# Kernel optimization log

Measured on AMD Instinct MI355X. Metric: run time of the kernel, lower is better.

The kernel has to match this reference:

```python
import jax, jax.numpy as jnp
import numpy as np

B, L, D, H = 4, 2048, 1024, 16
DH = D // H
EPS = 1e-6

def layer_norm(x, g, b):
    mu = jnp.mean(x, axis=-1, keepdims=True)
    var = jnp.mean(jnp.square(x - mu), axis=-1, keepdims=True)
    return (x - mu) * jax.lax.rsqrt(var + EPS) * g + b

def setup_inputs() -> dict:
    key = jax.random.key(0)
    ks = jax.random.split(key, 8)
    s = 0.02
    return {
        "x": jax.random.normal(ks[0], (B, L, D), jnp.float32),
        "mask": jnp.ones((B, L), jnp.int32),
        "Wq": jax.random.normal(ks[1], (D, D), jnp.float32) * s,
        "bq": jnp.zeros((D,), jnp.float32),
        "Wk": jax.random.normal(ks[2], (D, D), jnp.float32) * s,
        "bk": jnp.zeros((D,), jnp.float32),
        "Wv": jax.random.normal(ks[3], (D, D), jnp.float32) * s,
        "bv": jnp.zeros((D,), jnp.float32),
        "g1": jnp.ones((D,), jnp.float32),
        "b1": jnp.zeros((D,), jnp.float32),
        "g2": jnp.ones((D,), jnp.float32),
        "b2": jnp.zeros((D,), jnp.float32),
        "Wo1": jax.random.normal(ks[4], (D, D), jnp.float32) * s,
        "bo1": jnp.zeros((D,), jnp.float32),
        "Wo2": jax.random.normal(ks[5], (D, D), jnp.float32) * s,
        "bo2": jnp.zeros((D,), jnp.float32),
    }

def reference(x, mask, Wq, bq, Wk, bk, Wv, bv, g1, b1, g2, b2, Wo1, bo1, Wo2, bo2):
    h = layer_norm(x, g1, b1)                                  # [B,L,D]
    q = (h @ Wq + bq).reshape(B, L, H, DH)
    k = (h @ Wk + bk).reshape(B, L, H, DH)
    v = (h @ Wv + bv).reshape(B, L, H, DH)
    scores = jnp.einsum('bqhd,bkhd->bhqk', q, k) / jnp.sqrt(jnp.float32(DH))
    m = mask.astype(scores.dtype)[:, None, None, :]            # [B,1,1,L]
    scores = scores + (1.0 - m) * (-1e30)                      # mask_logits
    probs = jax.nn.softmax(scores, axis=-1)
    attn = jnp.einsum('bhqk,bkhd->bqhd', probs, v).reshape(B, L, D)
    residual = x + attn
    out = layer_norm(residual, g2, b2)
    out = jax.nn.gelu(out @ Wo1 + bo1, approximate=False)      # exact GELU (nn.GELU)
    out = out @ Wo2 + bo2 + residual
    return out
```

## Files before the change

kernel.cpp:

```cpp
#include <hip/hip_runtime.h>
#include <stdint.h>
#include <math.h>

typedef __bf16 bf16_t;
typedef __bf16 bf16x8 __attribute__((ext_vector_type(8)));
typedef __bf16 bf16x4 __attribute__((ext_vector_type(4)));
typedef float f32x4 __attribute__((ext_vector_type(4)));

#define B_ 4
#define L_ 2048
#define D_ 1024
#define H_ 16
#define DH_ 64
#define M_ (B_ * L_)
#define QSCALE 0.18033688011112042f

__device__ __forceinline__ void gload16(const bf16_t* gsrc, bf16_t* ldst) {
    __builtin_amdgcn_global_load_lds(
        (__attribute__((address_space(1))) void*)(void*)(gsrc),
        (__attribute__((address_space(3))) void*)(ldst), 16, 0, 0);
}

__device__ __forceinline__ float gelu_exact(float v) {
    return 0.5f * v * (1.0f + erff(v * 0.70710678118654752f));
}

__device__ __forceinline__ float fast_exp2(float x) {
#if __has_builtin(__builtin_amdgcn_exp2f)
    return __builtin_amdgcn_exp2f(x);
#else
    return exp2f(x);
#endif
}

__global__ __launch_bounds__(256) void transpose5(const float* __restrict__ W0, const float* __restrict__ W1,
                                                  const float* __restrict__ W2, const float* __restrict__ W3,
                                                  const float* __restrict__ W4,
                                                  bf16_t* __restrict__ T0, bf16_t* __restrict__ T1,
                                                  bf16_t* __restrict__ T2, bf16_t* __restrict__ T3,
                                                  bf16_t* __restrict__ T4) {
    const float* W; bf16_t* T;
    switch (blockIdx.z) {
        case 0: W = W0; T = T0; break;
        case 1: W = W1; T = T1; break;
        case 2: W = W2; T = T2; break;
        case 3: W = W3; T = T3; break;
        default: W = W4; T = T4; break;
    }
    __shared__ float tile[32][33];
    const int x = threadIdx.x, y0 = threadIdx.y;
    const int bx = blockIdx.x * 32, by = blockIdx.y * 32;
    for (int kk = 0; kk < 4; ++kk)
        tile[y0 + kk * 8][x] = W[(size_t)(by + y0 + kk * 8) * D_ + bx + x];
    __syncthreads();
    for (int kk = 0; kk < 4; ++kk)
        T[(size_t)(bx + y0 + kk * 8) * D_ + by + x] = (bf16_t)tile[x][y0 + kk * 8];
}

__global__ __launch_bounds__(256) void maskbias_kernel(const int* __restrict__ mask,
                                                       float* __restrict__ mb,
                                                       unsigned char* __restrict__ flags) {
    const int i = blockIdx.x * 256 + threadIdx.x;
    const int m = mask[i];
    mb[i] = m ? 0.f : -1.0e30f;
    const unsigned long long bal = __ballot(m != 0);
    __shared__ unsigned char ok[4];
    if ((threadIdx.x & 63) == 0) ok[threadIdx.x >> 6] = (bal == ~0ull) ? 1 : 0;
    __syncthreads();
    if (threadIdx.x < 2)
        flags[blockIdx.x * 2 + threadIdx.x] =
            (unsigned char)(ok[threadIdx.x * 2] & ok[threadIdx.x * 2 + 1]);
}

#define VTR_STRIDE 76
__global__ __launch_bounds__(256) void vtrans_kernel(const bf16_t* __restrict__ vb,
                                                     bf16_t* __restrict__ vt) {
    __shared__ bf16_t tile[128 * VTR_STRIDE];
    const int t = threadIdx.x;
    const int bh = blockIdx.y, b = bh >> 4, h = bh & 15;
    const int k0 = blockIdx.x * 128;
    #pragma unroll
    for (int it = 0; it < 4; ++it) {
        const int row = it * 32 + (t >> 3), c8 = (t & 7) * 8;
        *(uint4*)&tile[row * VTR_STRIDE + c8] =
            *(const uint4*)(vb + (size_t)(b * L_ + k0 + row) * D_ + h * DH_ + c8);
    }
    __syncthreads();
    #pragma unroll
    for (int it = 0; it < 4; ++it) {
        const int d = it * 16 + (t >> 4), pos0 = (t & 15) * 8;
        const int base32 = pos0 & ~31, g = (pos0 >> 3) & 3;
        union { uint4 u; bf16_t e[8]; } tv;
        #pragma unroll
        for (int j = 0; j < 8; ++j) {
            const int kk = base32 + ((j >> 2) << 4) + (g << 2) + (j & 3);
            tv.e[j] = tile[kk * VTR_STRIDE + d];
        }
        *(uint4*)&vt[((size_t)bh * DH_ + d) * L_ + k0 + pos0] = tv.u;
    }
}

__global__ __launch_bounds__(256) void ln1_kernel(const float* __restrict__ x,
                                                  const float* __restrict__ g,
                                                  const float* __restrict__ b,
                                                  bf16_t* __restrict__ h) {
    const int row = blockIdx.x, t = threadIdx.x;
    const float4 v = *(const float4*)(x + (size_t)row * D_ + t * 4);
    float s = v.x + v.y + v.z + v.w;
    float s2 = v.x * v.x + v.y * v.y + v.z * v.z + v.w * v.w;
    for (int m = 1; m < 64; m <<= 1) { s += __shfl_xor(s, m, 64); s2 += __shfl_xor(s2, m, 64); }
    __shared__ float red[2][4];
    if ((t & 63) == 0) { red[0][t >> 6] = s; red[1][t >> 6] = s2; }
    __syncthreads();
    s = red[0][0] + red[0][1] + red[0][2] + red[0][3];
    s2 = red[1][0] + red[1][1] + red[1][2] + red[1][3];
    const float mean = s * (1.f / 1024.f);
    const float var = s2 * (1.f / 1024.f) - mean * mean;
    const float rstd = rsqrtf(var + 1e-6f);
    const float4 gv = *(const float4*)(g + t * 4);
    const float4 bv = *(const float4*)(b + t * 4);
    union { bf16_t h4[4]; uint2 u; } o;
    o.h4[0] = (bf16_t)((v.x - mean) * rstd * gv.x + bv.x);
    o.h4[1] = (bf16_t)((v.y - mean) * rstd * gv.y + bv.y);
    o.h4[2] = (bf16_t)((v.z - mean) * rstd * gv.z + bv.z);
    o.h4[3] = (bf16_t)((v.w - mean) * rstd * gv.w + bv.w);
    *(uint2*)(h + (size_t)row * D_ + t * 4) = o.u;
}

__global__ __launch_bounds__(256) void add_ln2_kernel(const float* __restrict__ x,
                                                      const bf16_t* __restrict__ attnb,
                                                      const float* __restrict__ g,
                                                      const float* __restrict__ b,
                                                      bf16_t* __restrict__ residb,
                                                      bf16_t* __restrict__ h) {
    const int row = blockIdx.x, t = threadIdx.x;
    const float4 xv = *(const float4*)(x + (size_t)row * D_ + t * 4);
    union { uint2 u; bf16_t h4[4]; } ai;
    ai.u = *(const uint2*)(attnb + (size_t)row * D_ + t * 4);
    float4 v;
    v.x = xv.x + (float)ai.h4[0]; v.y = xv.y + (float)ai.h4[1];
    v.z = xv.z + (float)ai.h4[2]; v.w = xv.w + (float)ai.h4[3];
    union { bf16_t h4[4]; uint2 u; } rs;
    rs.h4[0] = (bf16_t)v.x; rs.h4[1] = (bf16_t)v.y; rs.h4[2] = (bf16_t)v.z; rs.h4[3] = (bf16_t)v.w;
    *(uint2*)(residb + (size_t)row * D_ + t * 4) = rs.u;
    float s = v.x + v.y + v.z + v.w;
    float s2 = v.x * v.x + v.y * v.y + v.z * v.z + v.w * v.w;
    for (int m = 1; m < 64; m <<= 1) { s += __shfl_xor(s, m, 64); s2 += __shfl_xor(s2, m, 64); }
    __shared__ float red[2][4];
    if ((t & 63) == 0) { red[0][t >> 6] = s; red[1][t >> 6] = s2; }
    __syncthreads();
    s = red[0][0] + red[0][1] + red[0][2] + red[0][3];
    s2 = red[1][0] + red[1][1] + red[1][2] + red[1][3];
    const float mean = s * (1.f / 1024.f);
    const float var = s2 * (1.f / 1024.f) - mean * mean;
    const float rstd = rsqrtf(var + 1e-6f);
    const float4 gv = *(const float4*)(g + t * 4);
    const float4 bv = *(const float4*)(b + t * 4);
    union { bf16_t h4[4]; uint2 u; } o;
    o.h4[0] = (bf16_t)((v.x - mean) * rstd * gv.x + bv.x);
    o.h4[1] = (bf16_t)((v.y - mean) * rstd * gv.y + bv.y);
    o.h4[2] = (bf16_t)((v.z - mean) * rstd * gv.z + bv.z);
    o.h4[3] = (bf16_t)((v.w - mean) * rstd * gv.w + bv.w);
    *(uint2*)(h + (size_t)row * D_ + t * 4) = o.u;
}

__global__ __launch_bounds__(256) void gemm_qkv(const bf16_t* __restrict__ A,
                                                const bf16_t* __restrict__ BT,
                                                const float* __restrict__ bq,
                                                const float* __restrict__ bk,
                                                const float* __restrict__ bv,
                                                bf16_t* __restrict__ qb,
                                                bf16_t* __restrict__ kb,
                                                bf16_t* __restrict__ vb) {
    constexpr int K = 1024;
    __shared__ bf16_t As[128 * 32];
    __shared__ bf16_t Bs[128 * 32];
    const int t = threadIdx.x;
    const int wave = t >> 6, lane = t & 63;
    const int l16 = lane & 15, g4 = lane >> 4;
    const int bm = blockIdx.x * 128, bn = blockIdx.y * 128;
    const int wm = (wave >> 1) * 64, wn = (wave & 1) * 64;

    f32x4 acc[4][4];
    for (int i = 0; i < 4; ++i)
        for (int j = 0; j < 4; ++j) acc[i][j] = (f32x4){0.f, 0.f, 0.f, 0.f};

    const int ar = t >> 2, ak = (t & 3) * 8;
    const bf16_t* Ag = A + (size_t)(bm + ar) * K + ak;
    const bf16_t* Bg = BT + (size_t)(bn + ar) * K + ak;
    bf16_t* Al = As + t * 8;
    bf16_t* Bl = Bs + t * 8;

    for (int kk = 0; kk < K; kk += 32) {
        __syncthreads();
        gload16(Ag + kk, Al);
        gload16(Ag + (size_t)64 * K + kk, Al + 2048);
        gload16(Bg + kk, Bl);
        gload16(Bg + (size_t)64 * K + kk, Bl + 2048);
        __syncthreads();
        bf16x8 af[4], bfr[4];
        for (int i = 0; i < 4; ++i)
            af[i] = *(const bf16x8*)&As[(wm + i * 16 + l16) * 32 + g4 * 8];
        for (int j = 0; j < 4; ++j)
            bfr[j] = *(const bf16x8*)&Bs[(wn + j * 16 + l16) * 32 + g4 * 8];
        for (int i = 0; i < 4; ++i)
            for (int j = 0; j < 4; ++j)
                acc[i][j] = __builtin_amdgcn_mfma_f32_16x16x32_bf16(af[i], bfr[j], acc[i][j], 0, 0, 0);
    }

    const int which = bn >> 10;
    const int c0 = bn & 1023;
    const float* bias = (which == 0) ? bq : (which == 1) ? bk : bv;
    bf16_t* ob = (which == 0) ? qb : (which == 1) ? kb : vb;
    const float scale = (which == 0) ? QSCALE : 1.0f;

    for (int i = 0; i < 4; ++i)
        for (int j = 0; j < 4; ++j) {
            const int col = c0 + wn + j * 16 + l16;
            const float bvv = bias[col];
            const int row0 = bm + wm + i * 16 + g4 * 4;
            for (int r = 0; r < 4; ++r) {
                const float vv = (acc[i][j][r] + bvv) * scale;
                ob[(size_t)(row0 + r) * D_ + col] = (bf16_t)vv;
            }
        }
}

template <int MODE>
__global__ __launch_bounds__(256) void gemm_bt(const bf16_t* __restrict__ A,
                                               const bf16_t* __restrict__ BT,
                                               const float* __restrict__ bias,
                                               const bf16_t* __restrict__ residb,
                                               bf16_t* __restrict__ outb,
                                               float* __restrict__ outf) {
    constexpr int K = 1024, N = 1024;
    __shared__ bf16_t As[128 * 32];
    __shared__ bf16_t Bs[128 * 32];
    const int t = threadIdx.x;
    const int wave = t >> 6, lane = t & 63;
    const int l16 = lane & 15, g4 = lane >> 4;
    const int bm = blockIdx.x * 128, bn = blockIdx.y * 128;
    const int wm = (wave >> 1) * 64, wn = (wave & 1) * 64;

    f32x4 acc[4][4];
    for (int i = 0; i < 4; ++i)
        for (int j = 0; j < 4; ++j) acc[i][j] = (f32x4){0.f, 0.f, 0.f, 0.f};

    const int ar = t >> 2, ak = (t & 3) * 8;
    const bf16_t* Ag = A + (size_t)(bm + ar) * K + ak;
    const bf16_t* Bg = BT + (size_t)(bn + ar) * K + ak;
    bf16_t* Al = As + t * 8;
    bf16_t* Bl = Bs + t * 8;

    for (int kk = 0; kk < K; kk += 32) {
        __syncthreads();
        gload16(Ag + kk, Al);
        gload16(Ag + (size_t)64 * K + kk, Al + 2048);
        gload16(Bg + kk, Bl);
        gload16(Bg + (size_t)64 * K + kk, Bl + 2048);
        __syncthreads();
        bf16x8 af[4], bfr[4];
        for (int i = 0; i < 4; ++i)
            af[i] = *(const bf16x8*)&As[(wm + i * 16 + l16) * 32 + g4 * 8];
        for (int j = 0; j < 4; ++j)
            bfr[j] = *(const bf16x8*)&Bs[(wn + j * 16 + l16) * 32 + g4 * 8];
        for (int i = 0; i < 4; ++i)
            for (int j = 0; j < 4; ++j)
                acc[i][j] = __builtin_amdgcn_mfma_f32_16x16x32_bf16(af[i], bfr[j], acc[i][j], 0, 0, 0);
    }

    for (int i = 0; i < 4; ++i)
        for (int j = 0; j < 4; ++j) {
            const int col = bn + wn + j * 16 + l16;
            const float bv = bias[col];
            const int row0 = bm + wm + i * 16 + g4 * 4;
            for (int r = 0; r < 4; ++r) {
                float vv = acc[i][j][r] + bv;
                const size_t idx = (size_t)(row0 + r) * N + col;
                if (MODE == 1) {
                    outb[idx] = (bf16_t)gelu_exact(vv);
                } else {
                    outf[idx] = vv + (float)residb[idx];
                }
            }
        }
}

#define VT_STRIDE 152
#define OS_STRIDE 72
__global__ __launch_bounds__(256, 3) void attn_kernel(const bf16_t* __restrict__ q,
                                                      const bf16_t* __restrict__ k,
                                                      const bf16_t* __restrict__ vt,
                                                      const float* __restrict__ maskbias,
                                                      const unsigned char* __restrict__ mflags,
                                                      bf16_t* __restrict__ attnb) {
    __shared__ bf16_t Ks[128 * 64];
    __shared__ bf16_t VT[64 * VT_STRIDE];
    bf16_t* Os = VT;

    const int t = threadIdx.x;
    const int wave = t >> 6, lane = t & 63;
    const int l16 = lane & 15, g4 = lane >> 4;
    const int id = blockIdx.x;
    const int xcd = id & 7, seq = id >> 3;
    const int bh = xcd * 8 + (seq >> 4);
    const int b = bh >> 4, h = bh & 15;
    const int q0 = (seq & 15) * 128;

    bf16x8 qf[2][2];
    for (int ti = 0; ti < 2; ++ti)
        for (int c = 0; c < 2; ++c)
            qf[ti][c] = *(const bf16x8*)(q + (size_t)(b * L_ + q0 + wave * 32 + ti * 16 + l16) * D_ +
                                         h * DH_ + c * 32 + g4 * 8);

    f32x4 accO[2][5];
    for (int ti = 0; ti < 2; ++ti)
        for (int dt = 0; dt < 5; ++dt) accO[ti][dt] = (f32x4){0.f, 0.f, 0.f, 0.f};

    const bf16_t ozv = (l16 == 0) ? (bf16_t)1.0f : (bf16_t)0.0f;
    const bf16x8 ones8 = (bf16x8){ozv, ozv, ozv, ozv, ozv, ozv, ozv, ozv};

    const int krow0 = t >> 3, kcg = t & 7;
    const int klcg = kcg ^ (krow0 & 7);
    const bf16_t* kbase = k + (size_t)(b * L_ + krow0) * D_ + h * DH_ + klcg * 8;
    bf16_t* kdst = Ks + t * 8;
    const int vrow0 = t >> 4, vkg = t & 15;
    const bf16_t* vbase = vt + ((size_t)bh * DH_ + vrow0) * L_ + vkg * 8;
    bf16_t* vdst = &VT[vrow0 * VT_STRIDE + vkg * 8];

    const int kb0 = l16 * 64 + ((g4 ^ (l16 & 7)) * 8);
    const int kb1 = l16 * 64 + (((g4 + 4) ^ (l16 & 7)) * 8);
    const int vrb = l16 * VT_STRIDE + g4 * 8;
    const unsigned char* flg = mflags + b * 16;

    for (int k0 = 0; k0 < L_; k0 += 128) {
        __syncthreads();
        #pragma unroll
        for (int it = 0; it < 4; ++it)
            gload16(kbase + (size_t)(k0 + it * 32) * D_, kdst + it * 2048);
        #pragma unroll
        for (int it = 0; it < 4; ++it) {
            const uint4 vv = *(const uint4*)(vbase + (size_t)(it * 16) * L_ + k0);
            *(uint4*)(vdst + it * 16 * VT_STRIDE) = vv;
        }
        __syncthreads();

        f32x4 s0[8], s1[8];
        #pragma unroll
        for (int tj = 0; tj < 8; ++tj) {
            const bf16x8 kf0 = *(const bf16x8*)&Ks[tj * 1024 + kb0];
            const bf16x8 kf1 = *(const bf16x8*)&Ks[tj * 1024 + kb1];
            f32x4 a = (f32x4){0.f, 0.f, 0.f, 0.f};
            a = __builtin_amdgcn_mfma_f32_16x16x32_bf16(kf0, qf[0][0], a, 0, 0, 0);
            a = __builtin_amdgcn_mfma_f32_16x16x32_bf16(kf1, qf[0][1], a, 0, 0, 0);
            s0[tj] = a;
            f32x4 a2 = (f32x4){0.f, 0.f, 0.f, 0.f};
            a2 = __builtin_amdgcn_mfma_f32_16x16x32_bf16(kf0, qf[1][0], a2, 0, 0, 0);
            a2 = __builtin_amdgcn_mfma_f32_16x16x32_bf16(kf1, qf[1][1], a2, 0, 0, 0);
            s1[tj] = a2;
        }

        if (!flg[k0 >> 7]) {
            #pragma unroll
            for (int tj = 0; tj < 8; ++tj) {
                const float4 mb = *(const float4*)&maskbias[b * L_ + k0 + tj * 16 + g4 * 4];
                s0[tj][0] += mb.x; s0[tj][1] += mb.y; s0[tj][2] += mb.z; s0[tj][3] += mb.w;
                s1[tj][0] += mb.x; s1[tj][1] += mb.y; s1[tj][2] += mb.z; s1[tj][3] += mb.w;
            }
        }

        bf16x8 pb0[4], pb1[4];
        #pragma unroll
        for (int c = 0; c < 4; ++c) {
            pb0[c] = (bf16x8){(bf16_t)fast_exp2(s0[2 * c][0]), (bf16_t)fast_exp2(s0[2 * c][1]),
                              (bf16_t)fast_exp2(s0[2 * c][2]), (bf16_t)fast_exp2(s0[2 * c][3]),
                              (bf16_t)fast_exp2(s0[2 * c + 1][0]), (bf16_t)fast_exp2(s0[2 * c + 1][1]),
                              (bf16_t)fast_exp2(s0[2 * c + 1][2]), (bf16_t)fast_exp2(s0[2 * c + 1][3])};
            pb1[c] = (bf16x8){(bf16_t)fast_exp2(s1[2 * c][0]), (bf16_t)fast_exp2(s1[2 * c][1]),
                              (bf16_t)fast_exp2(s1[2 * c][2]), (bf16_t)fast_exp2(s1[2 * c][3]),
                              (bf16_t)fast_exp2(s1[2 * c + 1][0]), (bf16_t)fast_exp2(s1[2 * c + 1][1]),
                              (bf16_t)fast_exp2(s1[2 * c + 1][2]), (bf16_t)fast_exp2(s1[2 * c + 1][3])};
        }

        #pragma unroll
        for (int c = 0; c < 4; ++c) {
            #pragma unroll
            for (int dt = 0; dt < 4; ++dt) {
                const bf16x8 va = *(const bf16x8*)&VT[vrb + dt * 16 * VT_STRIDE + c * 32];
                accO[0][dt] = __builtin_amdgcn_mfma_f32_16x16x32_bf16(va, pb0[c], accO[0][dt], 0, 0, 0);
                accO[1][dt] = __builtin_amdgcn_mfma_f32_16x16x32_bf16(va, pb1[c], accO[1][dt], 0, 0, 0);
            }
            accO[0][4] = __builtin_amdgcn_mfma_f32_16x16x32_bf16(ones8, pb0[c], accO[0][4], 0, 0, 0);
            accO[1][4] = __builtin_amdgcn_mfma_f32_16x16x32_bf16(ones8, pb1[c], accO[1][4], 0, 0, 0);
        }
    }

    __syncthreads();
    for (int ti = 0; ti < 2; ++ti) {
        const float lv = __shfl(accO[ti][4][0], l16, 64);
        const float rl = 1.0f / lv;
        #pragma unroll
        for (int dt = 0; dt < 4; ++dt) {
            bf16x4 o4 = (bf16x4){(bf16_t)(accO[ti][dt][0] * rl), (bf16_t)(accO[ti][dt][1] * rl),
                                 (bf16_t)(accO[ti][dt][2] * rl), (bf16_t)(accO[ti][dt][3] * rl)};
            *(bf16x4*)&Os[(wave * 32 + ti * 16 + l16) * OS_STRIDE + dt * 16 + g4 * 4] = o4;
        }
    }
    __syncthreads();
    for (int cc = 0; cc < 4; ++cc) {
        const int c2 = t + cc * 256;
        const int row = c2 >> 3, k8 = c2 & 7;
        const uint4 vv = *(const uint4*)&Os[row * OS_STRIDE + k8 * 8];
        *(uint4*)&attnb[(size_t)(b * L_ + q0 + row) * D_ + h * DH_ + k8 * 8] = vv;
    }
}

extern "C" void kernel_launch(void* const* d_in, const int* in_sizes, int n_in,
                              void* d_out, int out_size, void* d_ws, size_t ws_size,
                              hipStream_t stream) {
    const float* x    = (const float*)d_in[0];
    const int*   mask = (const int*)d_in[1];
    const float* Wq   = (const float*)d_in[2];
    const float* bq   = (const float*)d_in[3];
    const float* Wk   = (const float*)d_in[4];
    const float* bk   = (const float*)d_in[5];
    const float* Wv   = (const float*)d_in[6];
    const float* bv   = (const float*)d_in[7];
    const float* g1   = (const float*)d_in[8];
    const float* b1   = (const float*)d_in[9];
    const float* g2   = (const float*)d_in[10];
    const float* b2   = (const float*)d_in[11];
    const float* Wo1  = (const float*)d_in[12];
    const float* bo1  = (const float*)d_in[13];
    const float* Wo2  = (const float*)d_in[14];
    const float* bo2  = (const float*)d_in[15];

    char* ws = (char*)d_ws;
    const size_t MBs = 1ull << 20;
    bf16_t* WqkvT = (bf16_t*)(ws + 0 * MBs);
    bf16_t* Wo1T  = (bf16_t*)(ws + 6 * MBs);
    bf16_t* Wo2T  = (bf16_t*)(ws + 8 * MBs);
    bf16_t* h1    = (bf16_t*)(ws + 10 * MBs);
    bf16_t* vtb   = h1;
    bf16_t* qb    = (bf16_t*)(ws + 26 * MBs);
    bf16_t* kb    = (bf16_t*)(ws + 42 * MBs);
    bf16_t* vb    = (bf16_t*)(ws + 58 * MBs);
    bf16_t* attnb = (bf16_t*)(ws + 74 * MBs);
    bf16_t* residb= (bf16_t*)(ws + 90 * MBs);
    float*  mbias = (float*)(ws + 106 * MBs);
    unsigned char* mflags = (unsigned char*)(ws + 107 * MBs);
    bf16_t* h2    = qb;
    bf16_t* gact  = kb;

    transpose5<<<dim3(32, 32, 5), dim3(32, 8), 0, stream>>>(
        Wq, Wk, Wv, Wo1, Wo2,
        WqkvT, WqkvT + (size_t)D_ * D_, WqkvT + (size_t)2 * D_ * D_, Wo1T, Wo2T);

    maskbias_kernel<<<M_ / 256, 256, 0, stream>>>(mask, mbias, mflags);

    ln1_kernel<<<M_, 256, 0, stream>>>(x, g1, b1, h1);

    gemm_qkv<<<dim3(M_ / 128, 3 * D_ / 128), 256, 0, stream>>>(h1, WqkvT, bq, bk, bv, qb, kb, vb);

    vtrans_kernel<<<dim3(L_ / 128, B_ * H_), 256, 0, stream>>>(vb, vtb);

    attn_kernel<<<dim3(1024), 256, 0, stream>>>(qb, kb, vtb, mbias, mflags, attnb);

    add_ln2_kernel<<<M_, 256, 0, stream>>>(x, attnb, g2, b2, residb, h2);

    const dim3 gg(M_ / 128, D_ / 128);
    gemm_bt<1><<<gg, 256, 0, stream>>>(h2, Wo1T, bo1, nullptr, gact, nullptr);
    gemm_bt<2><<<gg, 256, 0, stream>>>(gact, Wo2T, bo2, residb, nullptr, (float*)d_out);
}
```

Before: 341.1 us.

## Merge prep kernels into one launch and swizzle attention V tile for occupancy

Folds the weight transpose, mask-bias and LN1 kernels into a single launch whose block index selects the task, removing two kernel launches and their serialization gaps. In the attention kernel, the padded V-transpose shared tile is replaced by an unpadded XOR-swizzled 128-wide layout, cutting shared memory to 32 KB. Launch bounds are raised from 3 to 4 blocks per CU to increase occupancy. The tighter register budget may cause spills, and the swizzle must keep bank conflicts low.

```diff
diff --git a/kernel.cpp b/kernel.cpp
--- a/kernel.cpp
+++ b/kernel.cpp
@@ -33,43 +33,73 @@
 #endif
 }
 
-__global__ __launch_bounds__(256) void transpose5(const float* __restrict__ W0, const float* __restrict__ W1,
-                                                  const float* __restrict__ W2, const float* __restrict__ W3,
-                                                  const float* __restrict__ W4,
-                                                  bf16_t* __restrict__ T0, bf16_t* __restrict__ T1,
-                                                  bf16_t* __restrict__ T2, bf16_t* __restrict__ T3,
-                                                  bf16_t* __restrict__ T4) {
-    const float* W; bf16_t* T;
-    switch (blockIdx.z) {
-        case 0: W = W0; T = T0; break;
-        case 1: W = W1; T = T1; break;
-        case 2: W = W2; T = T2; break;
-        case 3: W = W3; T = T3; break;
-        default: W = W4; T = T4; break;
-    }
-    __shared__ float tile[32][33];
-    const int x = threadIdx.x, y0 = threadIdx.y;
-    const int bx = blockIdx.x * 32, by = blockIdx.y * 32;
-    for (int kk = 0; kk < 4; ++kk)
-        tile[y0 + kk * 8][x] = W[(size_t)(by + y0 + kk * 8) * D_ + bx + x];
-    __syncthreads();
-    for (int kk = 0; kk < 4; ++kk)
-        T[(size_t)(bx + y0 + kk * 8) * D_ + by + x] = (bf16_t)tile[x][y0 + kk * 8];
-}
-
-__global__ __launch_bounds__(256) void maskbias_kernel(const int* __restrict__ mask,
-                                                       float* __restrict__ mb,
-                                                       unsigned char* __restrict__ flags) {
-    const int i = blockIdx.x * 256 + threadIdx.x;
-    const int m = mask[i];
-    mb[i] = m ? 0.f : -1.0e30f;
-    const unsigned long long bal = __ballot(m != 0);
-    __shared__ unsigned char ok[4];
-    if ((threadIdx.x & 63) == 0) ok[threadIdx.x >> 6] = (bal == ~0ull) ? 1 : 0;
-    __syncthreads();
-    if (threadIdx.x < 2)
-        flags[blockIdx.x * 2 + threadIdx.x] =
-            (unsigned char)(ok[threadIdx.x * 2] & ok[threadIdx.x * 2 + 1]);
+__global__ __launch_bounds__(256) void prep_kernel(const float* __restrict__ W0, const float* __restrict__ W1,
+                                                   const float* __restrict__ W2, const float* __restrict__ W3,
+                                                   const float* __restrict__ W4,
+                                                   bf16_t* __restrict__ T0, bf16_t* __restrict__ T1,
+                                                   bf16_t* __restrict__ T2, bf16_t* __restrict__ T3,
+                                                   bf16_t* __restrict__ T4,
+                                                   const int* __restrict__ mask,
+                                                   float* __restrict__ mb,
+                                                   unsigned char* __restrict__ flags,
+                                                   const float* __restrict__ x,
+                                                   const float* __restrict__ g1,
+                                                   const float* __restrict__ b1,
+                                                   bf16_t* __restrict__ h) {
+    const int z = blockIdx.x;
+    const int t = threadIdx.x;
+    if (z < 5120) {
+        const int wsel = z >> 10, tile = z & 1023;
+        const float* W; bf16_t* T;
+        switch (wsel) {
+            case 0: W = W0; T = T0; break;
+            case 1: W = W1; T = T1; break;
+            case 2: W = W2; T = T2; break;
+            case 3: W = W3; T = T3; break;
+            default: W = W4; T = T4; break;
+        }
+        __shared__ float tl[32][33];
+        const int xx = t & 31, y0 = t >> 5;
+        const int bx = (tile & 31) * 32, by = (tile >> 5) * 32;
+        for (int kk = 0; kk < 4; ++kk)
+            tl[y0 + kk * 8][xx] = W[(size_t)(by + y0 + kk * 8) * D_ + bx + xx];
+        __syncthreads();
+        for (int kk = 0; kk < 4; ++kk)
+            T[(size_t)(bx + y0 + kk * 8) * D_ + by + xx] = (bf16_t)tl[xx][y0 + kk * 8];
+    } else if (z < 5152) {
+        const int blk = z - 5120;
+        const int i = blk * 256 + t;
+        const int m = mask[i];
+        mb[i] = m ? 0.f : -1.0e30f;
+        const unsigned long long bal = __ballot(m != 0);
+        __shared__ unsigned char ok[4];
+        if ((t & 63) == 0) ok[t >> 6] = (bal == ~0ull) ? 1 : 0;
+        __syncthreads();
+        if (t < 2)
+            flags[blk * 2 + t] = (unsigned char)(ok[t * 2] & ok[t * 2 + 1]);
+    } else {
+        const int row = z - 5152;
+        const float4 v = *(const float4*)(x + (size_t)row * D_ + t * 4);
+        float s = v.x + v.y + v.z + v.w;
+        float s2 = v.x * v.x + v.y * v.y + v.z * v.z + v.w * v.w;
+        for (int m = 1; m < 64; m <<= 1) { s += __shfl_xor(s, m, 64); s2 += __shfl_xor(s2, m, 64); }
+        __shared__ float red[2][4];
+        if ((t & 63) == 0) { red[0][t >> 6] = s; red[1][t >> 6] = s2; }
+        __syncthreads();
+        s = red[0][0] + red[0][1] + red[0][2] + red[0][3];
+        s2 = red[1][0] + red[1][1] + red[1][2] + red[1][3];
+        const float mean = s * (1.f / 1024.f);
+        const float var = s2 * (1.f / 1024.f) - mean * mean;
+        const float rstd = rsqrtf(var + 1e-6f);
+        const float4 gv = *(const float4*)(g1 + t * 4);
+        const float4 bv = *(const float4*)(b1 + t * 4);
+        union { bf16_t h4[4]; uint2 u; } o;
+        o.h4[0] = (bf16_t)((v.x - mean) * rstd * gv.x + bv.x);
+        o.h4[1] = (bf16_t)((v.y - mean) * rstd * gv.y + bv.y);
+        o.h4[2] = (bf16_t)((v.z - mean) * rstd * gv.z + bv.z);
+        o.h4[3] = (bf16_t)((v.w - mean) * rstd * gv.w + bv.w);
+        *(uint2*)(h + (size_t)row * D_ + t * 4) = o.u;
+    }
 }
 
 #define VTR_STRIDE 76
@@ -98,33 +128,6 @@
         }
         *(uint4*)&vt[((size_t)bh * DH_ + d) * L_ + k0 + pos0] = tv.u;
     }
-}
-
-__global__ __launch_bounds__(256) void ln1_kernel(const float* __restrict__ x,
-                                                  const float* __restrict__ g,
-                                                  const float* __restrict__ b,
-                                                  bf16_t* __restrict__ h) {
-    const int row = blockIdx.x, t = threadIdx.x;
-    const float4 v = *(const float4*)(x + (size_t)row * D_ + t * 4);
-    float s = v.x + v.y + v.z + v.w;
-    float s2 = v.x * v.x + v.y * v.y + v.z * v.z + v.w * v.w;
-    for (int m = 1; m < 64; m <<= 1) { s += __shfl_xor(s, m, 64); s2 += __shfl_xor(s2, m, 64); }
-    __shared__ float red[2][4];
-    if ((t & 63) == 0) { red[0][t >> 6] = s; red[1][t >> 6] = s2; }
-    __syncthreads();
-    s = red[0][0] + red[0][1] + red[0][2] + red[0][3];
-    s2 = red[1][0] + red[1][1] + red[1][2] + red[1][3];
-    const float mean = s * (1.f / 1024.f);
-    const float var = s2 * (1.f / 1024.f) - mean * mean;
-    const float rstd = rsqrtf(var + 1e-6f);
-    const float4 gv = *(const float4*)(g + t * 4);
-    const float4 bv = *(const float4*)(b + t * 4);
-    union { bf16_t h4[4]; uint2 u; } o;
-    o.h4[0] = (bf16_t)((v.x - mean) * rstd * gv.x + bv.x);
-    o.h4[1] = (bf16_t)((v.y - mean) * rstd * gv.y + bv.y);
-    o.h4[2] = (bf16_t)((v.z - mean) * rstd * gv.z + bv.z);
-    o.h4[3] = (bf16_t)((v.w - mean) * rstd * gv.w + bv.w);
-    *(uint2*)(h + (size_t)row * D_ + t * 4) = o.u;
 }
 
 __global__ __launch_bounds__(256) void add_ln2_kernel(const float* __restrict__ x,
@@ -286,17 +289,17 @@
         }
 }
 
-#define VT_STRIDE 152
 #define OS_STRIDE 72
-__global__ __launch_bounds__(256, 3) void attn_kernel(const bf16_t* __restrict__ q,
+__global__ __launch_bounds__(256, 4) void attn_kernel(const bf16_t* __restrict__ q,
                                                       const bf16_t* __restrict__ k,
                                                       const bf16_t* __restrict__ vt,
                                                       const float* __restrict__ maskbias,
                                                       const unsigned char* __restrict__ mflags,
                                                       bf16_t* __restrict__ attnb) {
-    __shared__ bf16_t Ks[128 * 64];
-    __shared__ bf16_t VT[64 * VT_STRIDE];
-    bf16_t* Os = VT;
+    __shared__ char smem[32768];
+    bf16_t* Ks = (bf16_t*)smem;
+    bf16_t* VT = (bf16_t*)(smem + 16384);
+    bf16_t* Os = (bf16_t*)smem;
 
     const int t = threadIdx.x;
     const int wave = t >> 6, lane = t & 63;
@@ -326,11 +329,13 @@
     bf16_t* kdst = Ks + t * 8;
     const int vrow0 = t >> 4, vkg = t & 15;
     const bf16_t* vbase = vt + ((size_t)bh * DH_ + vrow0) * L_ + vkg * 8;
-    bf16_t* vdst = &VT[vrow0 * VT_STRIDE + vkg * 8];
+    bf16_t* vdst = &VT[vrow0 * 128 + (vkg ^ (vrow0 & 15)) * 8];
 
     const int kb0 = l16 * 64 + ((g4 ^ (l16 & 7)) * 8);
     const int kb1 = l16 * 64 + (((g4 + 4) ^ (l16 & 7)) * 8);
-    const int vrb = l16 * VT_STRIDE + g4 * 8;
+    int voff[4];
+    #pragma unroll
+    for (int c = 0; c < 4; ++c) voff[c] = l16 * 128 + (((c << 2) + g4) ^ l16) * 8;
     const unsigned char* flg = mflags + b * 16;
 
     for (int k0 = 0; k0 < L_; k0 += 128) {
@@ -341,7 +346,7 @@
         #pragma unroll
         for (int it = 0; it < 4; ++it) {
             const uint4 vv = *(const uint4*)(vbase + (size_t)(it * 16) * L_ + k0);
-            *(uint4*)(vdst + it * 16 * VT_STRIDE) = vv;
+            *(uint4*)(vdst + it * 16 * 128) = vv;
         }
         __syncthreads();
 
@@ -386,7 +391,7 @@
         for (int c = 0; c < 4; ++c) {
             #pragma unroll
             for (int dt = 0; dt < 4; ++dt) {
-                const bf16x8 va = *(const bf16x8*)&VT[vrb + dt * 16 * VT_STRIDE + c * 32];
+                const bf16x8 va = *(const bf16x8*)&VT[voff[c] + dt * 2048];
                 accO[0][dt] = __builtin_amdgcn_mfma_f32_16x16x32_bf16(va, pb0[c], accO[0][dt], 0, 0, 0);
                 accO[1][dt] = __builtin_amdgcn_mfma_f32_16x16x32_bf16(va, pb1[c], accO[1][dt], 0, 0, 0);
             }
@@ -452,13 +457,10 @@
     bf16_t* h2    = qb;
     bf16_t* gact  = kb;
 
-    transpose5<<<dim3(32, 32, 5), dim3(32, 8), 0, stream>>>(
+    prep_kernel<<<dim3(5120 + 32 + 8192), 256, 0, stream>>>(
         Wq, Wk, Wv, Wo1, Wo2,
-        WqkvT, WqkvT + (size_t)D_ * D_, WqkvT + (size_t)2 * D_ * D_, Wo1T, Wo2T);
-
-    maskbias_kernel<<<M_ / 256, 256, 0, stream>>>(mask, mbias, mflags);
-
-    ln1_kernel<<<M_, 256, 0, stream>>>(x, g1, b1, h1);
+        WqkvT, WqkvT + (size_t)D_ * D_, WqkvT + (size_t)2 * D_ * D_, Wo1T, Wo2T,
+        mask, mbias, mflags, x, g1, b1, h1);
 
     gemm_qkv<<<dim3(M_ / 128, 3 * D_ / 128), 256, 0, stream>>>(h1, WqkvT, bq, bk, bv, qb, kb, vb);
 
```

Result: slower. 385.3 us (+13.0%).
